# Performance work log

Measured on AMD Instinct MI355X. Metric: run time of the kernel, lower is better.

Reference implementation:

```python
import jax, jax.numpy as jnp
import numpy as np

N_TYPES = 10
BATCH = 16
SEQ = 512
STEPS = 10          # quadrature steps per interval (original hard-codes 10)
T_HORIZON = 100.0   # observation window end
T_MAX_EVENT = 90.0  # events strictly inside [0, T)


def setup_inputs() -> dict:
    key = jax.random.key(0)
    k1, k2, k3, k4, k5 = jax.random.split(key, 5)
    # sorted positive event times so the `times >= 0` filter in the original is a no-op
    event_times = jnp.sort(
        jax.random.uniform(k1, (BATCH, SEQ), dtype=jnp.float32) * T_MAX_EVENT, axis=1)
    event_types = jax.random.randint(k2, (BATCH, SEQ), 0, N_TYPES)
    # parameters, initialized exactly like _initialize_parameters()
    mu = jax.random.uniform(k3, (N_TYPES,), minval=0.01, maxval=0.1, dtype=jnp.float32)
    alpha = jax.random.uniform(k4, (N_TYPES, N_TYPES), minval=0.01, maxval=0.1, dtype=jnp.float32)
    beta = jax.random.uniform(k5, (N_TYPES, N_TYPES), minval=0.5, maxval=1.5, dtype=jnp.float32)
    T = jnp.asarray(T_HORIZON, dtype=jnp.float32)
    return {"event_times": event_times, "event_types": event_types, "T": T,
            "mu": mu, "alpha": alpha, "beta": beta}


def _hawkes_nll(event_times, event_types, T, mu, alpha, beta):
    B, S = event_times.shape
    dtype = event_times.dtype

    # ---- term 1: sum_i lambda_{type_i}(t_i | history) (original sums the raw
    # intensity, NOT its log -- reproduced faithfully) ----
    tj = event_types[:, None, :]            # past event type  (j axis)
    ti = event_types[:, :, None]            # current event type (i axis)
    dt = event_times[:, :, None] - event_times[:, None, :]   # [B, i, j] = t_i - t_j
    causal = jnp.arange(S)[:, None] > jnp.arange(S)[None, :]  # j < i
    dt_safe = jnp.where(causal[None], dt, 0.0)
    A = alpha[tj, ti]                        # alpha[type_j, type_i]  [B, S, S]
    Bm = beta[tj, ti]
    infl = jnp.where(causal[None], A * jnp.exp(-Bm * dt_safe), 0.0).sum(-1)  # [B, S]
    log_likelihood = (mu[event_types] + infl).sum()

    # ---- term 2: quadrature integral of total intensity over [0, T] ----
    # intervals: [0, t_1], [t_1, t_2], ..., [t_S, T]  -> S+1 intervals
    starts = jnp.concatenate([jnp.zeros((B, 1), dtype), event_times], axis=1)  # [B, S+1]
    ends = jnp.concatenate([event_times, jnp.broadcast_to(T, (B, 1)).astype(dtype)], axis=1)
    h = (ends - starts) / STEPS                                               # [B, S+1]
    # history for interval i is {j : t_j <= start_i} = {j < i} (sorted distinct times)
    hist = jnp.arange(S + 1)[:, None] > jnp.arange(S)[None, :]                # [S+1, S]
    arow = alpha[event_types]                # alpha[type_j, :]  [B, S, K]
    brow = beta[event_types]                 # beta[type_j, :]   [B, S, K]

    acc = jnp.zeros((B, S + 1), dtype)       # sum over quadrature points of influence
    for p in range(STEPS + 1):
        tp = starts + p * h                                                   # [B, S+1]
        dtp = jnp.where(hist[None], tp[:, :, None] - event_times[:, None, :], 0.0)  # [B,S+1,S]
        dec = jnp.exp(-brow[:, None] * dtp[..., None])                        # [B,S+1,S,K]
        acc = acc + jnp.where(hist[None, :, :, None], arow[:, None] * dec, 0.0).sum((2, 3))
    # each of the STEPS+1 quadrature points also contributes mu.sum()
    vals = acc + (STEPS + 1) * mu.sum()
    integral = (vals * h).sum()

    return -(log_likelihood - integral)


def reference(event_times, event_types, T, mu, alpha, beta):
    return _hawkes_nll(event_times, event_types, T, mu, alpha, beta)
```

## Files before the change

### kernel.cpp

```cpp
#include <hip/hip_runtime.h>

#define NT     10
#define NBATCH 16
#define SEQ    512
#define KSTEPS 10
#define NC     16
#define CL     (SEQ / NC)


__global__ __launch_bounds__(128) void hawkes_chunk(
    const float* __restrict__ times, const int* __restrict__ types,
    const float* __restrict__ Tptr,  const float* __restrict__ mu,
    const float* __restrict__ alpha, const float* __restrict__ beta,
    float4* __restrict__ p4, float2* __restrict__ p2,
    float* __restrict__ out)
{
    __shared__ float s_t[CL + 1];
    __shared__ int   s_ty[CL];

    const int blk = blockIdx.x;
    const int t   = threadIdx.x;
    const int b   = blk / NC;
    const int c   = blk - b * NC;
    const int k0  = c * CL;

    if (blk == 0 && t == 0) out[0] = 0.f;

    const float* bt  = times + b * SEQ;
    const int*   bty = types + b * SEQ;
    if (t <= CL) { const int j = k0 - 1 + t; s_t[t] = (j >= 0) ? bt[j] : 0.f; }
    if (t < CL)  s_ty[t] = bty[k0 + t];
    __syncthreads();

    const int a = t / NT;
    const int m = t - a * NT;
    const bool active = (t < NT * NT);
    float al = 0.f, be = 0.f, mum = 0.f;
    if (active) {
        al  = alpha[a * NT + m];
        be  = beta [a * NT + m];
        mum = (a == 0) ? mu[m] : 0.f;
    }

    float A = 1.f, gl = 0.f, C = 0.f, D = 0.f, E = 0.f, F = 0.f;
    float tprev = s_t[0];

    #pragma unroll 8
    for (int i = 0; i < CL; ++i) {
        const float te   = s_t[i + 1];
        const float h    = (te - tprev) * (1.0f / KSTEPS);
        tprev = te;
        const float x    = be * h;
        const float e1   = __expf(-x);
        const float e10  = __expf(-10.f * x);
        const float gA   = (1.f - e10 * e1) * __builtin_amdgcn_rcpf(1.f - e1);
        const float gB   = 11.f + x * (-55.f + 192.5f * x);
        const float geom = (x > 1e-3f) ? gA : gB;
        const float coef = al * geom * h;
        C = fmaf(coef, A,  C);
        D = fmaf(coef, gl, D);
        A  *= e10;
        gl *= e10;
        const int ty = s_ty[i];
        E  = (ty == m) ? fmaf(al, A,  E) : E;
        F  = (ty == m) ? (F + fmaf(al, gl, mum)) : F;
        gl += (ty == a) ? 1.f : 0.f;
    }
    if (c == NC - 1) {
        const float h    = (Tptr[0] - tprev) * (1.0f / KSTEPS);
        const float x    = be * h;
        const float e1   = __expf(-x);
        const float e10  = __expf(-10.f * x);
        const float gA   = (1.f - e10 * e1) * __builtin_amdgcn_rcpf(1.f - e1);
        const float gB   = 11.f + x * (-55.f + 192.5f * x);
        const float geom = (x > 1e-3f) ? gA : gB;
        const float coef = al * geom * h;
        C = fmaf(coef, A,  C);
        D = fmaf(coef, gl, D);
    }

    const int slot = blk * 128 + t;
    p4[slot] = make_float4(A, gl, C, D);
    p2[slot] = make_float2(E, F);
}

__global__ __launch_bounds__(128) void hawkes_fold(
    const float4* __restrict__ p4, const float2* __restrict__ p2,
    const float* __restrict__ mu, const float* __restrict__ Tptr,
    float* __restrict__ out)
{
    const int b = blockIdx.x;
    const int t = threadIdx.x;

    float g = 0.f, I = 0.f, Lk = 0.f;
    #pragma unroll
    for (int c = 0; c < NC; ++c) {
        const int slot = (b * NC + c) * 128 + t;
        const float4 v = p4[slot];
        const float2 w = p2[slot];
        I  += fmaf(v.z, g, v.w);
        Lk += fmaf(w.x, g, w.y);
        g   = fmaf(v.x, g, v.y);
    }

    float S = I - Lk;
    for (int off = 32; off; off >>= 1) S += __shfl_down(S, off);

    __shared__ float red[2];
    const int w = t >> 6, ln = t & 63;
    if (ln == 0) red[w] = S;
    __syncthreads();
    if (t == 0) {
        float mus = 0.f;
        #pragma unroll
        for (int i = 0; i < NT; ++i) mus += mu[i];
        const float cst = (float)(KSTEPS + 1) * mus * Tptr[0] * (1.0f / KSTEPS);
        atomicAdd(out, red[0] + red[1] + cst);
    }
}

extern "C" void kernel_launch(void* const* d_in, const int* in_sizes, int n_in,
                              void* d_out, int out_size, void* d_ws, size_t ws_size,
                              hipStream_t stream) {
    const float* times = (const float*)d_in[0];
    const int*   types = (const int*)d_in[1];
    const float* T     = (const float*)d_in[2];
    const float* mu    = (const float*)d_in[3];
    const float* alpha = (const float*)d_in[4];
    const float* beta  = (const float*)d_in[5];

    const int nslots = NBATCH * NC * 128;
    float4* p4 = (float4*)d_ws;
    float2* p2 = (float2*)((char*)d_ws + (size_t)nslots * sizeof(float4));
    float*  out = (float*)d_out;

    hawkes_chunk<<<NBATCH * NC, 128, 0, stream>>>(times, types, T, mu, alpha, beta,
                                                  p4, p2, out);
    hawkes_fold<<<NBATCH, 128, 0, stream>>>(p4, p2, mu, T, out);
}
```

Baseline: 11.97 us.

## Fuse chunk and fold kernels into one block-local scan over type-pair slices

Replaces the two-kernel chunk/fold pipeline with a single kernel where each block handles one batch and a fifth of the type pairs across all 16 chunks. The per-chunk affine summaries are combined through shared memory instead of a global workspace, which removes the second kernel launch and the global round trip. Zeroing the output moves to a hipMemsetAsync, which adds a separate stream operation. The grid shrinks from 256 blocks of 128 threads to 80 blocks of 320 threads, with less wasted lane work but fewer blocks spread across CUs.

```diff
diff --git a/kernel.cpp b/kernel.cpp
--- a/kernel.cpp
+++ b/kernel.cpp
@@ -1,53 +1,55 @@
 #include <hip/hip_runtime.h>
 
-#define NT     10
-#define NBATCH 16
-#define SEQ    512
-#define KSTEPS 10
-#define NC     16
-#define CL     (SEQ / NC)
+#define NT      10
+#define NBATCH  16
+#define SEQ     512
+#define KSTEPS  10
+#define NC      16
+#define CL      (SEQ / NC)
+#define SPLIT   5
+#define SPB     (NT * NT / SPLIT)
+#define THREADS (NC * SPB)
 
 
-__global__ __launch_bounds__(128) void hawkes_chunk(
+__global__ __launch_bounds__(THREADS) void hawkes_fused(
     const float* __restrict__ times, const int* __restrict__ types,
     const float* __restrict__ Tptr,  const float* __restrict__ mu,
     const float* __restrict__ alpha, const float* __restrict__ beta,
-    float4* __restrict__ p4, float2* __restrict__ p2,
     float* __restrict__ out)
 {
-    __shared__ float s_t[CL + 1];
-    __shared__ int   s_ty[CL];
+    __shared__ float s_time[SEQ];
+    __shared__ int   s_ty[SEQ];
+    __shared__ float cA[NC][SPB], cB[NC][SPB], cC[NC][SPB],
+                     cD[NC][SPB], cE[NC][SPB], cF[NC][SPB];
+    __shared__ float s_part[SPB];
 
     const int blk = blockIdx.x;
+    const int b   = blk / SPLIT;
+    const int sp  = blk - b * SPLIT;
     const int t   = threadIdx.x;
-    const int b   = blk / NC;
-    const int c   = blk - b * NC;
-    const int k0  = c * CL;
-
-    if (blk == 0 && t == 0) out[0] = 0.f;
 
     const float* bt  = times + b * SEQ;
     const int*   bty = types + b * SEQ;
-    if (t <= CL) { const int j = k0 - 1 + t; s_t[t] = (j >= 0) ? bt[j] : 0.f; }
-    if (t < CL)  s_ty[t] = bty[k0 + t];
+    #pragma unroll
+    for (int i = t; i < SEQ; i += THREADS) { s_time[i] = bt[i]; s_ty[i] = bty[i]; }
     __syncthreads();
 
-    const int a = t / NT;
-    const int m = t - a * NT;
-    const bool active = (t < NT * NT);
-    float al = 0.f, be = 0.f, mum = 0.f;
-    if (active) {
-        al  = alpha[a * NT + m];
-        be  = beta [a * NT + m];
-        mum = (a == 0) ? mu[m] : 0.f;
-    }
+    const int c  = t / SPB;
+    const int sl = t - c * SPB;
+    const int s  = sp * SPB + sl;
+    const int a  = s / NT;
+    const int m  = s - a * NT;
+    const float al  = alpha[a * NT + m];
+    const float be  = beta [a * NT + m];
+    const float mum = (a == 0) ? mu[m] : 0.f;
 
-    float A = 1.f, gl = 0.f, C = 0.f, D = 0.f, E = 0.f, F = 0.f;
-    float tprev = s_t[0];
+    float A = 1.f, gl = 0.f, C_ = 0.f, D = 0.f, E = 0.f, F = 0.f;
+    const int k0 = c * CL;
+    float tprev = (c == 0) ? 0.f : s_time[k0 - 1];
 
     #pragma unroll 8
     for (int i = 0; i < CL; ++i) {
-        const float te   = s_t[i + 1];
+        const float te   = s_time[k0 + i];
         const float h    = (te - tprev) * (1.0f / KSTEPS);
         tprev = te;
         const float x    = be * h;
@@ -57,11 +59,11 @@
         const float gB   = 11.f + x * (-55.f + 192.5f * x);
         const float geom = (x > 1e-3f) ? gA : gB;
         const float coef = al * geom * h;
-        C = fmaf(coef, A,  C);
-        D = fmaf(coef, gl, D);
+        C_ = fmaf(coef, A,  C_);
+        D  = fmaf(coef, gl, D);
         A  *= e10;
         gl *= e10;
-        const int ty = s_ty[i];
+        const int ty = s_ty[k0 + i];
         E  = (ty == m) ? fmaf(al, A,  E) : E;
         F  = (ty == m) ? (F + fmaf(al, gl, mum)) : F;
         gl += (ty == a) ? 1.f : 0.f;
@@ -75,47 +77,37 @@
         const float gB   = 11.f + x * (-55.f + 192.5f * x);
         const float geom = (x > 1e-3f) ? gA : gB;
         const float coef = al * geom * h;
-        C = fmaf(coef, A,  C);
-        D = fmaf(coef, gl, D);
+        C_ = fmaf(coef, A,  C_);
+        D  = fmaf(coef, gl, D);
     }
 
-    const int slot = blk * 128 + t;
-    p4[slot] = make_float4(A, gl, C, D);
-    p2[slot] = make_float2(E, F);
-}
+    cA[c][sl] = A;  cB[c][sl] = gl;
+    cC[c][sl] = C_; cD[c][sl] = D;
+    cE[c][sl] = E;  cF[c][sl] = F;
+    __syncthreads();
 
-__global__ __launch_bounds__(128) void hawkes_fold(
-    const float4* __restrict__ p4, const float2* __restrict__ p2,
-    const float* __restrict__ mu, const float* __restrict__ Tptr,
-    float* __restrict__ out)
-{
-    const int b = blockIdx.x;
-    const int t = threadIdx.x;
-
-    float g = 0.f, I = 0.f, Lk = 0.f;
-    #pragma unroll
-    for (int c = 0; c < NC; ++c) {
-        const int slot = (b * NC + c) * 128 + t;
-        const float4 v = p4[slot];
-        const float2 w = p2[slot];
-        I  += fmaf(v.z, g, v.w);
-        Lk += fmaf(w.x, g, w.y);
-        g   = fmaf(v.x, g, v.y);
+    if (t < SPB) {
+        float g = 0.f, I = 0.f, Lk = 0.f;
+        #pragma unroll
+        for (int cc = 0; cc < NC; ++cc) {
+            I  += fmaf(cC[cc][t], g, cD[cc][t]);
+            Lk += fmaf(cE[cc][t], g, cF[cc][t]);
+            g   = fmaf(cA[cc][t], g, cB[cc][t]);
+        }
+        s_part[t] = I - Lk;
     }
-
-    float S = I - Lk;
-    for (int off = 32; off; off >>= 1) S += __shfl_down(S, off);
-
-    __shared__ float red[2];
-    const int w = t >> 6, ln = t & 63;
-    if (ln == 0) red[w] = S;
     __syncthreads();
     if (t == 0) {
-        float mus = 0.f;
+        float S = 0.f;
         #pragma unroll
-        for (int i = 0; i < NT; ++i) mus += mu[i];
-        const float cst = (float)(KSTEPS + 1) * mus * Tptr[0] * (1.0f / KSTEPS);
-        atomicAdd(out, red[0] + red[1] + cst);
+        for (int i = 0; i < SPB; ++i) S += s_part[i];
+        if (sp == 0) {
+            float mus = 0.f;
+            #pragma unroll
+            for (int i = 0; i < NT; ++i) mus += mu[i];
+            S += (float)(KSTEPS + 1) * mus * Tptr[0] * (1.0f / KSTEPS);
+        }
+        atomicAdd(out, S);
     }
 }
 
@@ -128,13 +120,9 @@
     const float* mu    = (const float*)d_in[3];
     const float* alpha = (const float*)d_in[4];
     const float* beta  = (const float*)d_in[5];
+    float* out = (float*)d_out;
 
-    const int nslots = NBATCH * NC * 128;
-    float4* p4 = (float4*)d_ws;
-    float2* p2 = (float2*)((char*)d_ws + (size_t)nslots * sizeof(float4));
-    float*  out = (float*)d_out;
-
-    hawkes_chunk<<<NBATCH * NC, 128, 0, stream>>>(times, types, T, mu, alpha, beta,
-                                                  p4, p2, out);
-    hawkes_fold<<<NBATCH, 128, 0, stream>>>(p4, p2, mu, T, out);
+    hipMemsetAsync(out, 0, sizeof(float), stream);
+    hawkes_fused<<<NBATCH * SPLIT, THREADS, 0, stream>>>(times, types, T, mu,
+                                                         alpha, beta, out);
 }
```

Measured after the change: 16.42 us. 37.1% more time.
